# Performance work log

Measured on AMD Instinct MI355X. Metric: run time of the kernel, lower is better.

Reference implementation:

```python
import jax, jax.numpy as jnp
from jax import lax
import numpy as np

QMIN, QMAX = -127.0, 127.0
STRIDE = (1, 1)
PADDING = ((1, 1), (1, 1))
DILATION = (1, 1)
DN = ('NCHW', 'OIHW', 'NCHW')


def _quantize_x(x, scale_x):
    # symmetric static per-tensor int8 quantization
    return jnp.clip(jnp.round(x / scale_x), QMIN, QMAX)


def _quantize_w(w):
    # symmetric dynamic per-output-channel int8 quantization
    scale_w = jnp.max(jnp.abs(w), axis=(1, 2, 3), keepdims=True) / QMAX  # [O,1,1,1]
    q_w = jnp.clip(jnp.round(w / scale_w), QMIN, QMAX)
    return q_w, scale_w


def setup_inputs() -> dict:
    key = jax.random.key(0)
    kx, kw, kb = jax.random.split(key, 3)
    B, C, H, W = 32, 128, 56, 56
    O, kH, kW = 256, 3, 3
    x = jax.random.normal(kx, (B, C, H, W), jnp.float32)
    weight = jax.random.normal(kw, (O, C, kH, kW), jnp.float32) * 0.05
    bias = jax.random.normal(kb, (O,), jnp.float32)
    scale_x = jnp.asarray(0.02, jnp.float32)  # static per-tensor scale buffer
    # exact int8 product lookup table: lut[a+127, b+127] = a*b
    v = np.arange(-127, 128, dtype=np.int32)
    lut = jnp.asarray(v[:, None] * v[None, :])
    return {"x": x, "weight": weight, "bias": bias, "scale_x": scale_x, "lut": lut}


def reference(x, weight, bias, scale_x, lut):
    # lut holds the exact int8 product table, so bgemm_int8(q_x, q_w, lut) is an
    # exact integer GEMM; im2col + bGEMM == conv of quantized tensors.
    q_x = _quantize_x(x, scale_x)            # [B,C,H,W] integer-valued fp32
    q_w, scale_w = _quantize_w(weight)       # [O,C,kH,kW], [O,1,1,1]
    acc = lax.conv_general_dilated(
        q_x, q_w, STRIDE, PADDING, rhs_dilation=DILATION, dimension_numbers=DN
    )                                        # [B,O,OH,OW] integer-valued accumulator
    out = acc * scale_x * scale_w.reshape(1, -1, 1, 1)  # per-channel dequant
    return out + bias.reshape(1, -1, 1, 1)
```

## Files before the change

### kernel.cpp

```cpp
#include <hip/hip_runtime.h>


#define BATCH 32
#define CIN   128
#define HH    56
#define WW    56
#define OCH   256

typedef __attribute__((ext_vector_type(4))) int int4v;

#define QX_BYTES (32 * 56 * 56 * 128)
#define QW_BYTES (256 * 1152)
#define WS_NEEDED (QX_BYTES + QW_BYTES + 1024)

__device__ __forceinline__ void gload_lds16(const void* g, void* l) {
  __builtin_amdgcn_global_load_lds(
      (const __attribute__((address_space(1))) unsigned int*)g,
      (__attribute__((address_space(3))) unsigned int*)l, 16, 0, 0);
}

__global__ __launch_bounds__(256) void quant_w_kernel(
    const float* __restrict__ w, const float* __restrict__ sxp,
    char* __restrict__ qwf, float* __restrict__ alpha) {
  __shared__ float wf[1152];
  __shared__ float red[256];
  const int o = blockIdx.x;
  const int tid = threadIdx.x;
  const float* wrow = w + (size_t)o * 1152;
  float m = 0.f;
  for (int i = tid; i < 288; i += 256) {
    const float4 v = ((const float4*)wrow)[i];
    ((float4*)wf)[i] = v;
    m = fmaxf(m, fmaxf(fmaxf(fabsf(v.x), fabsf(v.y)),
                       fmaxf(fabsf(v.z), fabsf(v.w))));
  }
  red[tid] = m;
  __syncthreads();
  for (int s = 128; s > 0; s >>= 1) {
    if (tid < s) red[tid] = fmaxf(red[tid], red[tid + s]);
    __syncthreads();
  }
  const float sc = red[0] / 127.0f;
  if (tid == 0) alpha[o] = sc * sxp[0];
  if (tid < 36) {
    const int r = tid >> 2, c04 = tid & 3;
    const int og = o >> 5, t = (o >> 4) & 1, l16 = o & 15;
    unsigned int* dst = (unsigned int*)(qwf + (size_t)og * 36864 +
                                        ((r * 4 + c04) * 2 + t) * 512 + l16 * 32);
#pragma unroll
    for (int g = 0; g < 8; ++g) {
      unsigned int pk = 0;
#pragma unroll
      for (int k = 0; k < 4; ++k) {
        const int c = c04 * 32 + g * 4 + k;
        const int q = (int)fminf(127.f, fmaxf(-127.f, rintf(wf[c * 9 + r] / sc)));
        pk |= ((unsigned int)(q & 255)) << (8 * k);
      }
      dst[g] = pk;
    }
  }
}

__global__ __launch_bounds__(256) void quant_x_kernel(
    const float* __restrict__ x, const float* __restrict__ sxp,
    unsigned int* __restrict__ qxp) {
  __shared__ char ldsA[128 * 60];
  const int row = blockIdx.x;
  const int b = row / 56, h = row % 56;
  const float sx = sxp[0];
  for (int i = threadIdx.x; i < 1792; i += 256) {
    const int c = i / 14, f = i % 14;
    const float4 v =
        *(const float4*)(x + (((size_t)b * 128 + c) * 56 + h) * 56 + 4 * f);
    unsigned int pk;
    pk  = (unsigned int)((int)fminf(127.f, fmaxf(-127.f, rintf(v.x / sx))) & 255);
    pk |= ((unsigned int)((int)fminf(127.f, fmaxf(-127.f, rintf(v.y / sx))) & 255)) << 8;
    pk |= ((unsigned int)((int)fminf(127.f, fmaxf(-127.f, rintf(v.z / sx))) & 255)) << 16;
    pk |= ((unsigned int)((int)fminf(127.f, fmaxf(-127.f, rintf(v.w / sx))) & 255)) << 24;
    *(unsigned int*)(ldsA + c * 60 + 4 * f) = pk;
  }
  __syncthreads();
  unsigned int* orow = qxp + (size_t)row * 56 * 32;
  for (int i = threadIdx.x; i < 1792; i += 256) {
    const int w = i >> 5, jd = i & 31;
    const int c0 = (jd ^ (((w + 1) & 15) << 1)) << 2;
    unsigned int pk = 0;
#pragma unroll
    for (int k = 0; k < 4; ++k)
      pk |= ((unsigned int)(unsigned char)ldsA[(c0 + k) * 60 + w]) << (8 * k);
    orow[i] = pk;
  }
}

#define XSLAB 8448

__global__ __launch_bounds__(256, 6) void conv_kernel(
    const char* __restrict__ qxp, const char* __restrict__ qwf,
    const float* __restrict__ alpha, const float* __restrict__ bias,
    float* __restrict__ out) {
  __shared__ __attribute__((aligned(16))) char Xs8[3 * XSLAB];

  const int bi = blockIdx.x;
  const int b  = bi / 56;
  const int oh = bi % 56;
  const int o0 = blockIdx.y * 128;
  const int tid = threadIdx.x;
  const int wave = tid >> 6, lane = tid & 63;
  const int l16 = lane & 15, quad = lane >> 4;

  int m_r[4], n_r[4];
  {
    int4v zz = {0, 0, 0, 0};
    long a1 = 0, b1 = 0, a2 = 0, b2 = 0;
    if (quad == 0) {
      a1 = 1L;
      b1 = (long)(l16 + 1);
      a2 = (long)(l16 + 1);
      b2 = 1L;
    }
    int4v d1 = __builtin_amdgcn_mfma_i32_16x16x32_i8(a1, b1, zz, 0, 0, 0);
    int4v d2 = __builtin_amdgcn_mfma_i32_16x16x32_i8(a2, b2, zz, 0, 0, 0);
#pragma unroll
    for (int r = 0; r < 4; ++r) {
      n_r[r] = (d1[r] - 1) & 15;
      m_r[r] = (d2[r] - 1) & 15;
    }
  }

  for (int kh = 0; kh < 3; ++kh) {
    const int ih = oh - 1 + kh;
    char* slab = Xs8 + kh * XSLAB;
    if (ih >= 0 && ih < HH) {
      const char* src = qxp + ((size_t)b * 56 + ih) * 7168;
      for (int i = tid; i < 448; i += 256)
        gload_lds16(src + i * 16, slab + 128 + i * 16);
      for (int i = tid; i < 320; i += 256) {
        const int cg = i >> 5, dw = i & 31;
        const int col = (cg == 0) ? 0 : 56 + cg;
        ((unsigned int*)slab)[col * 32 + dw] = 0u;
      }
    } else {
      for (int i = tid; i < 2112; i += 256) ((unsigned int*)slab)[i] = 0u;
    }
  }

  int4v acc[2][4];
#pragma unroll
  for (int t = 0; t < 2; ++t)
#pragma unroll
    for (int u = 0; u < 4; ++u) acc[t][u] = (int4v){0, 0, 0, 0};

  __syncthreads();

  const long* wbase = (const long*)qwf +
      (size_t)(blockIdx.y * 4 + wave) * 4608 + (l16 * 4 + quad);

#pragma unroll
  for (int kh = 0; kh < 3; ++kh) {
    const char* Xk = Xs8 + kh * XSLAB;
#pragma unroll
    for (int kw = 0; kw < 3; ++kw) {
      const int ph = ((l16 + kw) & 15) << 3;
#pragma unroll
      for (int c04 = 0; c04 < 4; ++c04) {
        const int fi = ((kh * 3 + kw) * 4 + c04) * 2;
        const long aop0 = wbase[(size_t)fi * 64];
        const long aop1 = wbase[(size_t)fi * 64 + 64];
        const int boff = (c04 * 32 + quad * 8) ^ ph;
        long bop[4];
#pragma unroll
        for (int u = 0; u < 4; ++u)
          bop[u] = *(const long*)(Xk + (u * 16 + l16 + kw) * 128 + boff);
#pragma unroll
        for (int u = 0; u < 4; ++u) {
          acc[0][u] = __builtin_amdgcn_mfma_i32_16x16x32_i8(
              aop0, bop[u], acc[0][u], 0, 0, 0);
          acc[1][u] = __builtin_amdgcn_mfma_i32_16x16x32_i8(
              aop1, bop[u], acc[1][u], 0, 0, 0);
        }
      }
    }
  }

#pragma unroll
  for (int t = 0; t < 2; ++t) {
#pragma unroll
    for (int u = 0; u < 4; ++u) {
#pragma unroll
      for (int r = 0; r < 4; ++r) {
        const int ol = wave * 32 + t * 16 + m_r[r];
        const int ow = u * 16 + n_r[r];
        if (ow < WW) {
          const int oo = o0 + ol;
          out[(((size_t)b * OCH + oo) * HH + oh) * WW + ow] =
              (float)acc[t][u][r] * alpha[oo] + bias[oo];
        }
      }
    }
  }
}

#define FAS_ROW 392
#define FXS_ROW 136
#define FLDS_XS (128 * FAS_ROW)
#define FLDS_SC (FLDS_XS + 66 * FXS_ROW)
#define FLDS_AL (FLDS_SC + 512)
#define FLDS_BI (FLDS_AL + 512)
#define FLDS_RED (FLDS_BI + 512)
#define FLDS_TOT (FLDS_RED + 1024)

__global__ __launch_bounds__(256) void conv_fused_kernel(
    const float* __restrict__ x, const float* __restrict__ w,
    const float* __restrict__ bias, const float* __restrict__ sxp,
    float* __restrict__ out) {
  __shared__ __attribute__((aligned(16))) char lds[FLDS_TOT];
  char* As8 = lds;
  char* Xs8 = lds + FLDS_XS;
  float* scaleS = (float*)(lds + FLDS_SC);
  float* alphaS = (float*)(lds + FLDS_AL);
  float* biasS  = (float*)(lds + FLDS_BI);
  float* red    = (float*)(lds + FLDS_RED);

  const int bi = blockIdx.x;
  const int b  = bi / 56;
  const int oh = bi % 56;
  const int o0 = blockIdx.y * 128;
  const int tid = threadIdx.x;
  const int wave = tid >> 6, lane = tid & 63;
  const int l16 = lane & 15, quad = lane >> 4;
  const float sx = sxp[0];

  int m_r[4], n_r[4];
  {
    int4v zz = {0, 0, 0, 0};
    long a1 = 0, b1 = 0, a2 = 0, b2 = 0;
    if (quad == 0) { a1 = 1L; b1 = (long)(l16 + 1); a2 = (long)(l16 + 1); b2 = 1L; }
    int4v d1 = __builtin_amdgcn_mfma_i32_16x16x32_i8(a1, b1, zz, 0, 0, 0);
    int4v d2 = __builtin_amdgcn_mfma_i32_16x16x32_i8(a2, b2, zz, 0, 0, 0);
#pragma unroll
    for (int r = 0; r < 4; ++r) { n_r[r] = (d1[r] - 1) & 15; m_r[r] = (d2[r] - 1) & 15; }
  }
  {
    const int o = tid >> 1, half = tid & 1;
    const float4* p = (const float4*)(w + (size_t)(o0 + o) * 1152 + half * 576);
    float m = 0.f;
#pragma unroll 4
    for (int i = 0; i < 144; ++i) {
      const float4 v = p[i];
      m = fmaxf(m, fmaxf(fmaxf(fabsf(v.x), fabsf(v.y)), fmaxf(fabsf(v.z), fabsf(v.w))));
    }
    red[tid] = m;
  }
  __syncthreads();
  {
    const int o = tid >> 1;
    if ((tid & 1) == 0) {
      const float sc = fmaxf(red[2 * o], red[2 * o + 1]) / 127.0f;
      scaleS[o] = sc; alphaS[o] = sc * sx; biasS[o] = bias[o0 + o];
    }
  }
  int4v acc[2][4];
#pragma unroll
  for (int t = 0; t < 2; ++t)
#pragma unroll
    for (int u = 0; u < 4; ++u) acc[t][u] = (int4v){0, 0, 0, 0};

  for (int kh = 0; kh < 3; ++kh) {
    const int ih = oh - 1 + kh;
    const bool row_ok = (ih >= 0) && (ih < HH);
    __syncthreads();
    for (int idx = tid; idx < 66 * 128; idx += 256) {
      const int col = idx % 66, c = idx / 66, iw = col - 1;
      int q = 0;
      if (row_ok && iw >= 0 && iw < WW) {
        const float xv = x[(((size_t)b * CIN + c) * HH + ih) * WW + iw];
        q = (int)fminf(127.f, fmaxf(-127.f, rintf(xv / sx)));
      }
      Xs8[col * FXS_ROW + c] = (char)q;
    }
    for (int idx = tid; idx < 16384; idx += 256) {
      const int c = idx & 127, o = idx >> 7;
      const float s = scaleS[o];
      const float* wp = w + (size_t)(o0 + o) * 1152 + c * 9 + kh * 3;
#pragma unroll
      for (int kw = 0; kw < 3; ++kw) {
        const int q = (int)fminf(127.f, fmaxf(-127.f, rintf(wp[kw] / s)));
        As8[o * FAS_ROW + kw * 128 + c] = (char)q;
      }
    }
    __syncthreads();
    const int obase = wave * 32;
#pragma unroll
    for (int kw = 0; kw < 3; ++kw) {
#pragma unroll
      for (int c0 = 0; c0 < 128; c0 += 32) {
        long aop[2], bop[4];
#pragma unroll
        for (int t = 0; t < 2; ++t)
          aop[t] = *(const long*)(As8 + (obase + t * 16 + l16) * FAS_ROW + kw * 128 + c0 + quad * 8);
#pragma unroll
        for (int u = 0; u < 4; ++u)
          bop[u] = *(const long*)(Xs8 + (u * 16 + l16 + kw) * FXS_ROW + c0 + quad * 8);
#pragma unroll
        for (int t = 0; t < 2; ++t)
#pragma unroll
          for (int u = 0; u < 4; ++u)
            acc[t][u] = __builtin_amdgcn_mfma_i32_16x16x32_i8(aop[t], bop[u], acc[t][u], 0, 0, 0);
      }
    }
  }
#pragma unroll
  for (int t = 0; t < 2; ++t) {
#pragma unroll
    for (int u = 0; u < 4; ++u) {
#pragma unroll
      for (int r = 0; r < 4; ++r) {
        const int ol = wave * 32 + t * 16 + m_r[r];
        const int ow = u * 16 + n_r[r];
        if (ow < WW)
          out[(((size_t)b * OCH + o0 + ol) * HH + oh) * WW + ow] =
              (float)acc[t][u][r] * alphaS[ol] + biasS[ol];
      }
    }
  }
}

extern "C" void kernel_launch(void* const* d_in, const int* in_sizes, int n_in,
                              void* d_out, int out_size, void* d_ws, size_t ws_size,
                              hipStream_t stream) {
  const float *x = nullptr, *w = nullptr, *bias = nullptr, *sx = nullptr;
  for (int i = 0; i < n_in; ++i) {
    const int s = in_sizes[i];
    if (s == BATCH * CIN * HH * WW) x = (const float*)d_in[i];
    else if (s == OCH * CIN * 9)    w = (const float*)d_in[i];
    else if (s == OCH)              bias = (const float*)d_in[i];
    else if (s == 1)                sx = (const float*)d_in[i];
  }
  if (!x || !w || !bias || !sx) {
    x = (const float*)d_in[0]; w = (const float*)d_in[1];
    bias = (const float*)d_in[2]; sx = (const float*)d_in[3];
  }
  float* out = (float*)d_out;

  if (ws_size >= (size_t)WS_NEEDED) {
    unsigned int* qxp = (unsigned int*)d_ws;
    char* qwf = (char*)d_ws + QX_BYTES;
    float* alpha = (float*)((char*)d_ws + QX_BYTES + QW_BYTES);
    quant_w_kernel<<<OCH, 256, 0, stream>>>(w, sx, qwf, alpha);
    quant_x_kernel<<<BATCH * HH, 256, 0, stream>>>(x, sx, qxp);
    conv_kernel<<<dim3(BATCH * HH, 2), 256, 0, stream>>>(
        (const char*)qxp, qwf, alpha, bias, out);
  } else {
    conv_fused_kernel<<<dim3(BATCH * HH, 2), 256, 0, stream>>>(x, w, bias, sx, out);
  }
}
```

Before: 224.8 us.

## Interleave weight layout, prefetch weights across taps, remap blocks per XCD

Repacks quantized weights so the two 16-channel halves for a lane are adjacent, which lets the conv kernel fetch both A operands with one 16-byte load. Weight loads for the next filter tap are double-buffered in registers and issued before the current tap's MFMAs, hiding global latency. The grid is flattened and remapped so consecutive rows of the same image (which share input slabs) land on the same XCD for L2 reuse. The cost is more registers held for the prefetch buffers, which may reduce occupancy.

```diff
diff --git a/kernel.cpp b/kernel.cpp
--- a/kernel.cpp
+++ b/kernel.cpp
@@ -8,6 +8,7 @@
 #define OCH   256
 
 typedef __attribute__((ext_vector_type(4))) int int4v;
+typedef __attribute__((ext_vector_type(2))) long longx2;
 
 #define QX_BYTES (32 * 56 * 56 * 128)
 #define QW_BYTES (256 * 1152)
@@ -45,18 +46,22 @@
   if (tid < 36) {
     const int r = tid >> 2, c04 = tid & 3;
     const int og = o >> 5, t = (o >> 4) & 1, l16 = o & 15;
-    unsigned int* dst = (unsigned int*)(qwf + (size_t)og * 36864 +
-                                        ((r * 4 + c04) * 2 + t) * 512 + l16 * 32);
-#pragma unroll
-    for (int g = 0; g < 8; ++g) {
-      unsigned int pk = 0;
-#pragma unroll
-      for (int k = 0; k < 4; ++k) {
-        const int c = c04 * 32 + g * 4 + k;
-        const int q = (int)fminf(127.f, fmaxf(-127.f, rintf(wf[c * 9 + r] / sc)));
-        pk |= ((unsigned int)(q & 255)) << (8 * k);
-      }
-      dst[g] = pk;
+    unsigned int* base = (unsigned int*)(qwf + (size_t)og * 36864 +
+                                         (size_t)(r * 4 + c04) * 1024);
+#pragma unroll
+    for (int quad = 0; quad < 4; ++quad) {
+#pragma unroll
+      for (int half = 0; half < 2; ++half) {
+        unsigned int pk = 0;
+#pragma unroll
+        for (int k = 0; k < 4; ++k) {
+          const int c = c04 * 32 + quad * 8 + half * 4 + k;
+          const int q =
+              (int)fminf(127.f, fmaxf(-127.f, rintf(wf[c * 9 + r] / sc)));
+          pk |= ((unsigned int)(q & 255)) << (8 * k);
+        }
+        base[(l16 * 4 + quad) * 4 + t * 2 + half] = pk;
+      }
     }
   }
 }
@@ -100,10 +105,15 @@
     float* __restrict__ out) {
   __shared__ __attribute__((aligned(16))) char Xs8[3 * XSLAB];
 
-  const int bi = blockIdx.x;
+  const int id = blockIdx.x;
+  const int xcd = id & 7;
+  int kk = id >> 3;
+  const int yy = (kk >= 224) ? 1 : 0;
+  kk -= yy * 224;
+  const int bi = xcd * 224 + kk;
   const int b  = bi / 56;
   const int oh = bi % 56;
-  const int o0 = blockIdx.y * 128;
+  const int o0 = yy * 128;
   const int tid = threadIdx.x;
   const int wave = tid >> 6, lane = tid & 63;
   const int l16 = lane & 15, quad = lane >> 4;
@@ -126,6 +136,12 @@
       m_r[r] = (d2[r] - 1) & 15;
     }
   }
+
+  const longx2* wb2 = (const longx2*)(qwf + (size_t)(yy * 4 + wave) * 36864) +
+                      (l16 * 4 + quad);
+  longx2 ap[2][4];
+#pragma unroll
+  for (int c04 = 0; c04 < 4; ++c04) ap[0][c04] = wb2[(size_t)c04 * 64];
 
   for (int kh = 0; kh < 3; ++kh) {
     const int ih = oh - 1 + kh;
@@ -152,32 +168,29 @@
 
   __syncthreads();
 
-  const long* wbase = (const long*)qwf +
-      (size_t)(blockIdx.y * 4 + wave) * 4608 + (l16 * 4 + quad);
-
-#pragma unroll
-  for (int kh = 0; kh < 3; ++kh) {
+#pragma unroll
+  for (int g = 0; g < 9; ++g) {
+    const int kh = g / 3, kw = g % 3;
+    if (g < 8) {
+#pragma unroll
+      for (int c04 = 0; c04 < 4; ++c04)
+        ap[(g + 1) & 1][c04] = wb2[(size_t)((g + 1) * 4 + c04) * 64];
+    }
     const char* Xk = Xs8 + kh * XSLAB;
-#pragma unroll
-    for (int kw = 0; kw < 3; ++kw) {
-      const int ph = ((l16 + kw) & 15) << 3;
-#pragma unroll
-      for (int c04 = 0; c04 < 4; ++c04) {
-        const int fi = ((kh * 3 + kw) * 4 + c04) * 2;
-        const long aop0 = wbase[(size_t)fi * 64];
-        const long aop1 = wbase[(size_t)fi * 64 + 64];
-        const int boff = (c04 * 32 + quad * 8) ^ ph;
-        long bop[4];
-#pragma unroll
-        for (int u = 0; u < 4; ++u)
-          bop[u] = *(const long*)(Xk + (u * 16 + l16 + kw) * 128 + boff);
-#pragma unroll
-        for (int u = 0; u < 4; ++u) {
-          acc[0][u] = __builtin_amdgcn_mfma_i32_16x16x32_i8(
-              aop0, bop[u], acc[0][u], 0, 0, 0);
-          acc[1][u] = __builtin_amdgcn_mfma_i32_16x16x32_i8(
-              aop1, bop[u], acc[1][u], 0, 0, 0);
-        }
+    const int ph = ((l16 + kw) & 15) << 3;
+#pragma unroll
+    for (int c04 = 0; c04 < 4; ++c04) {
+      const int boff = (c04 * 32 + quad * 8) ^ ph;
+      long bop[4];
+#pragma unroll
+      for (int u = 0; u < 4; ++u)
+        bop[u] = *(const long*)(Xk + (u * 16 + l16 + kw) * 128 + boff);
+#pragma unroll
+      for (int u = 0; u < 4; ++u) {
+        acc[0][u] = __builtin_amdgcn_mfma_i32_16x16x32_i8(
+            ap[g & 1][c04][0], bop[u], acc[0][u], 0, 0, 0);
+        acc[1][u] = __builtin_amdgcn_mfma_i32_16x16x32_i8(
+            ap[g & 1][c04][1], bop[u], acc[1][u], 0, 0, 0);
       }
     }
   }
@@ -348,7 +361,7 @@
     float* alpha = (float*)((char*)d_ws + QX_BYTES + QW_BYTES);
     quant_w_kernel<<<OCH, 256, 0, stream>>>(w, sx, qwf, alpha);
     quant_x_kernel<<<BATCH * HH, 256, 0, stream>>>(x, sx, qxp);
-    conv_kernel<<<dim3(BATCH * HH, 2), 256, 0, stream>>>(
+    conv_kernel<<<BATCH * HH * 2, 256, 0, stream>>>(
         (const char*)qxp, qwf, alpha, bias, out);
   } else {
     conv_fused_kernel<<<dim3(BATCH * HH, 2), 256, 0, stream>>>(x, w, bias, sx, out);
```

New measurement: 196.9 us. 1.14x faster.
